# Kernel tuning notes

Hardware: AMD Instinct MI355X
Metric: run time of the kernel (lower is better)

Reference implementation:

```python
import jax, jax.numpy as jnp
import numpy as np

N_EMBD = 2048
N_Q = 32
N_KV = 8
GROUP = N_Q // N_KV   # 4
HD = N_EMBD // N_Q    # 64
BASE = 10000.0
NEG_INF = -1e30


def _rope(x):
    """Rotate-half RoPE on last dim; positions 1..t along dim -2 (as in the
    original _build_cache which uses arange(1, seq_len+1))."""
    t, d = x.shape[-2], x.shape[-1]
    d2 = d // 2
    theta = 1.0 / (BASE ** (jnp.arange(0, d, 2, dtype=jnp.float32) / d))  # (d/2,)
    pos = jnp.arange(1, t + 1, dtype=jnp.float32)                          # (t,)
    ang = pos[:, None] * theta[None, :]                                    # (t, d/2)
    ang = jnp.concatenate([ang, ang], axis=-1)                             # (t, d)
    sin, cos = jnp.sin(ang), jnp.cos(ang)
    rot = jnp.concatenate([-x[..., d2:], x[..., :d2]], axis=-1)
    return x * cos + rot * sin


def setup_inputs() -> dict:
    key = jax.random.key(0)
    ks = jax.random.split(key, 5)
    b, t = 2, 1024
    s = 1.0 / np.sqrt(N_EMBD)
    return {
        "x": jax.random.normal(ks[0], (b, t, N_EMBD), dtype=jnp.float32),
        "wq": jax.random.normal(ks[1], (N_EMBD, N_EMBD), dtype=jnp.float32) * s,
        "bq": jnp.zeros((N_EMBD,), dtype=jnp.float32),
        "wk": jax.random.normal(ks[2], (N_EMBD, N_KV * HD), dtype=jnp.float32) * s,
        "bk": jnp.zeros((N_KV * HD,), dtype=jnp.float32),
        "wv": jax.random.normal(ks[3], (N_EMBD, N_KV * HD), dtype=jnp.float32) * s,
        "bv": jnp.zeros((N_KV * HD,), dtype=jnp.float32),
        "wo": jax.random.normal(ks[4], (N_EMBD, N_EMBD), dtype=jnp.float32) * s,
        "bo": jnp.zeros((N_EMBD,), dtype=jnp.float32),
    }


def reference(x, wq, bq, wk, bk, wv, bv, wo, bo):
    b, t, _ = x.shape
    q = x @ wq + bq                                   # (b, t, E)
    k = x @ wk + bk                                   # (b, t, NKV*HD)
    v = x @ wv + bv
    q = q.reshape(b, t, N_Q, HD).transpose(0, 2, 1, 3)        # (b, nq, t, d)
    q = q.reshape(b, N_KV, GROUP, t, HD)                      # (b, hkv, g, t, d)
    k = k.reshape(b, t, N_KV, HD).transpose(0, 2, 1, 3)       # (b, hkv, t, d)
    v = v.reshape(b, t, N_KV, HD).transpose(0, 2, 1, 3)
    q = _rope(q)
    k = _rope(k)
    scale = jnp.sqrt(jnp.float32(HD))
    att = jnp.einsum("bhgqd,bhkd->bhgqk", q, k) / scale       # (b, hkv, g, t, t)
    causal = jnp.tril(jnp.ones((t, t), dtype=bool))
    att = jnp.where(causal, att, NEG_INF)
    att = jax.nn.softmax(att, axis=-1)
    out = jnp.einsum("bhgqk,bhkd->bhgqd", att, v)             # (b, hkv, g, t, d)
    out = out.transpose(0, 3, 1, 2, 4).reshape(b, t, N_EMBD)  # (b, t, E)
    return out @ wo + bo
```

## Files before the change

kernel.cpp:

```cpp
#include <hip/hip_runtime.h>
#include <hip/hip_bf16.h>
#include <cstdint>


typedef __attribute__((ext_vector_type(8))) short short8;
typedef __attribute__((ext_vector_type(4))) short short4v;
typedef __attribute__((ext_vector_type(4))) float f32x4;

__device__ inline short f2b(float f) {
  union { float f; unsigned u; } v; v.f = f;
  unsigned r = v.u + 0x7fffu + ((v.u >> 16) & 1u);
  return (short)(r >> 16);
}

__device__ inline float exp2_fast(float x) {
  float r;
  asm("v_exp_f32 %0, %1" : "=v"(r) : "v"(x));
  return r;
}

__device__ inline void gl_lds16(const void* g, void* l) {
  __builtin_amdgcn_global_load_lds((const __attribute__((address_space(1))) void*)g,
                                   (__attribute__((address_space(3))) void*)l,
                                   16, 0, 0);
}

__global__ void cast_x_kernel(const float* __restrict__ x, short* __restrict__ xb, int n4) {
  int i = blockIdx.x * 256 + threadIdx.x;
  if (i >= n4) return;
  float4 v = ((const float4*)x)[i];
  short4v o; o.x = f2b(v.x); o.y = f2b(v.y); o.z = f2b(v.z); o.w = f2b(v.w);
  ((short4v*)xb)[i] = o;
}

__global__ void wtrans_all(const float* __restrict__ wq, const float* __restrict__ wk,
                           const float* __restrict__ wv, const float* __restrict__ wo,
                           short* __restrict__ WqkvT, short* __restrict__ woT) {
  __shared__ float tile[64][65];
  const int bx = blockIdx.x;
  const float* W; short* WT; int N, off, nb;
  if (bx < 32)      { W = wq; WT = WqkvT; N = 2048; off = 0;    nb = bx * 64; }
  else if (bx < 40) { W = wk; WT = WqkvT; N = 512;  off = 2048; nb = (bx - 32) * 64; }
  else if (bx < 48) { W = wv; WT = WqkvT; N = 512;  off = 2560; nb = (bx - 40) * 64; }
  else              { W = wo; WT = woT;   N = 2048; off = 0;    nb = (bx - 48) * 64; }
  const int kb = blockIdx.y * 64;
  const int tid = threadIdx.x;
  const int c = tid & 63, r0 = tid >> 6;
#pragma unroll
  for (int s = 0; s < 16; ++s) {
    int k = r0 + s * 4;
    tile[c][k] = W[(size_t)(kb + k) * N + nb + c];
  }
  __syncthreads();
#pragma unroll
  for (int s = 0; s < 16; ++s) {
    int n = r0 + s * 4;
    WT[(size_t)(off + nb + n) * 2048 + kb + c] = f2b(tile[n][c]);
  }
}

__device__ __forceinline__ void gemm_loop_bk64(const short* __restrict__ Ag,
                                               const short* __restrict__ Bg,
                                               short* lA, short* lB,
                                               int w, int l15, int q4,
                                               f32x4 acc[2][4]) {
  const int K = 2048, NS = 32;
  auto stage = [&](int s, int d) {
    const short* As = Ag + s * 64;
    const short* Bs = Bg + s * 64;
    short* a = lA + d * 8192 + w * 512;
    gl_lds16(As, a);
    gl_lds16(As + 64 * K, a + 2048);
    gl_lds16(As + 32, a + 4096);
    gl_lds16(As + 64 * K + 32, a + 6144);
    short* bp = lB + d * 4096 + w * 512;
    gl_lds16(Bs, bp);
    gl_lds16(Bs + 32, bp + 2048);
  };
  stage(0, 0);
  for (int s = 0; s < NS; ++s) {
    const int d = s & 1;
    __syncthreads();
    if (s + 1 < NS) stage(s + 1, d ^ 1);
#pragma unroll
    for (int ks = 0; ks < 2; ++ks) {
      const short* ap = lA + d * 8192 + ks * 4096;
      const short* bp = lB + d * 4096 + ks * 2048;
      short8 af[2], bf[4];
#pragma unroll
      for (int mf = 0; mf < 2; ++mf) af[mf] = *(const short8*)(ap + (w * 32 + mf * 16 + l15) * 32 + q4 * 8);
#pragma unroll
      for (int nf = 0; nf < 4; ++nf) bf[nf] = *(const short8*)(bp + (nf * 16 + l15) * 32 + q4 * 8);
#pragma unroll
      for (int mf = 0; mf < 2; ++mf)
#pragma unroll
        for (int nf = 0; nf < 4; ++nf)
          acc[mf][nf] = __builtin_amdgcn_mfma_f32_16x16x32_bf16(af[mf], bf[nf], acc[mf][nf], 0, 0, 0);
    }
  }
}

__launch_bounds__(256, 3)
__global__ void gemm_qkv(const short* __restrict__ A, const short* __restrict__ BT,
                         const float* __restrict__ bq, const float* __restrict__ bk,
                         const float* __restrict__ bv,
                         short* __restrict__ Qb, short* __restrict__ Kb,
                         short* __restrict__ Vtd) {
  __shared__ __align__(16) short lA[16384];
  __shared__ __align__(16) short lB[8192];
  const int K = 2048;
  const int tid = threadIdx.x, lane = tid & 63, w = tid >> 6;
  const int q4 = lane >> 4, l15 = lane & 15;
  const int bn = blockIdx.x * 64, bm = blockIdx.y * 128;

  const short* Ag = A + (size_t)(bm + (tid >> 2)) * K + ((tid & 3) << 3);
  const short* Bg = BT + (size_t)(bn + (tid >> 2)) * K + ((tid & 3) << 3);

  f32x4 acc[2][4];
  const f32x4 fz = {0.f, 0.f, 0.f, 0.f};
#pragma unroll
  for (int i = 0; i < 2; ++i)
#pragma unroll
    for (int j = 0; j < 4; ++j) acc[i][j] = fz;

  gemm_loop_bk64(Ag, Bg, lA, lB, w, l15, q4, acc);

  const float L2T = 0.4152410118609203f;
  const float theta_a = exp2_fast(-(float)l15 * L2T);
  const float theta_b = exp2_fast(-(float)(l15 + 16) * L2T);
  const float s2 = 0.18033688011112042f;

  if (bn < 2048) {
    const int h = bn >> 6;
    float bb0 = bq[bn + l15], bb1 = bq[bn + 16 + l15], bb2 = bq[bn + 32 + l15], bb3 = bq[bn + 48 + l15];
#pragma unroll
    for (int mf = 0; mf < 2; ++mf)
#pragma unroll
      for (int r = 0; r < 4; ++r) {
        int row = bm + w * 32 + mf * 16 + q4 * 4 + r;
        int batch = row >> 10, t = row & 1023;
        float pos = (float)(t + 1);
        float sa, ca, sb, cb;
        __sincosf(pos * theta_a, &sa, &ca);
        __sincosf(pos * theta_b, &sb, &cb);
        float x0 = acc[mf][0][r] + bb0, x2 = acc[mf][2][r] + bb2;
        float x1 = acc[mf][1][r] + bb1, x3 = acc[mf][3][r] + bb3;
        size_t base = ((size_t)(batch * 32 + h) * 1024 + t) * 64;
        Qb[base + l15]      = f2b((x0 * ca - x2 * sa) * s2);
        Qb[base + l15 + 32] = f2b((x2 * ca + x0 * sa) * s2);
        Qb[base + l15 + 16] = f2b((x1 * cb - x3 * sb) * s2);
        Qb[base + l15 + 48] = f2b((x3 * cb + x1 * sb) * s2);
      }
  } else if (bn < 2560) {
    const int co = bn - 2048;
    const int hkv = co >> 6;
    float bb0 = bk[co + l15], bb1 = bk[co + 16 + l15], bb2 = bk[co + 32 + l15], bb3 = bk[co + 48 + l15];
#pragma unroll
    for (int mf = 0; mf < 2; ++mf)
#pragma unroll
      for (int r = 0; r < 4; ++r) {
        int row = bm + w * 32 + mf * 16 + q4 * 4 + r;
        int batch = row >> 10, t = row & 1023;
        float pos = (float)(t + 1);
        float sa, ca, sb, cb;
        __sincosf(pos * theta_a, &sa, &ca);
        __sincosf(pos * theta_b, &sb, &cb);
        float x0 = acc[mf][0][r] + bb0, x2 = acc[mf][2][r] + bb2;
        float x1 = acc[mf][1][r] + bb1, x3 = acc[mf][3][r] + bb3;
        size_t base = (size_t)(batch * 8 + hkv) * 65536 + t * 32;
        Kb[base + l15]              = f2b(x0 * ca - x2 * sa);
        Kb[base + l15 + 16]         = f2b(x1 * cb - x3 * sb);
        Kb[base + 32768 + l15]      = f2b(x2 * ca + x0 * sa);
        Kb[base + 32768 + l15 + 16] = f2b(x3 * cb + x1 * sb);
      }
  } else {
    const int co = bn - 2560;
    const int hkv = co >> 6;
    float bb[4];
#pragma unroll
    for (int nf = 0; nf < 4; ++nf) bb[nf] = bv[co + nf * 16 + l15];
#pragma unroll
    for (int mf = 0; mf < 2; ++mf)
#pragma unroll
      for (int r = 0; r < 4; ++r) {
        int row = bm + w * 32 + mf * 16 + q4 * 4 + r;
        int batch = row >> 10, t = row & 1023;
        size_t base = (size_t)(batch * 8 + hkv) * 65536 + (size_t)t * 64;
#pragma unroll
        for (int nf = 0; nf < 4; ++nf)
          Vtd[base + nf * 16 + l15] = f2b(acc[mf][nf][r] + bb[nf]);
      }
  }
}

__global__ void vtrans2_kernel(const short* __restrict__ Vtd, short* __restrict__ VTb) {
  __shared__ short tile[64][72];
  const int tt = blockIdx.x, h = blockIdx.y, b = blockIdx.z;
  const int tid = threadIdx.x;
  const size_t base = (size_t)(b * 8 + h) * 65536;
#pragma unroll
  for (int p = 0; p < 2; ++p) {
    int r = (tid >> 3) + p * 32;
    int c0 = (tid & 7) * 8;
    short8 v = *(const short8*)(Vtd + base + (size_t)(tt * 64 + r) * 64 + c0);
#pragma unroll
    for (int j = 0; j < 8; ++j) tile[c0 + j][r] = v[j];
  }
  __syncthreads();
  const int d = tid >> 2, ts = (tid & 3) * 8;
#pragma unroll
  for (int tc = 0; tc < 2; ++tc) {
    short8 v = *(const short8*)(&tile[d][tc * 32 + ts]);
    *(short8*)(VTb + base + (size_t)(tt * 2 + tc) * 2048 + d * 32 + ts) = v;
  }
}

#define PROW 72
__launch_bounds__(256, 3)
__global__ void attn5_kernel(const short* __restrict__ Qb, const short* __restrict__ Kb,
                             const short* __restrict__ VTb, short* __restrict__ AO) {
  __shared__ __align__(16) short lK[2][128 * 32];
  __shared__ __align__(16) short lVT[4][64 * 32];
  __shared__ __align__(16) short lP[4][2][16 * PROW];
  const int tid = threadIdx.x, lane = tid & 63, w = tid >> 6;
  const int q4 = lane >> 4, l15 = lane & 15;
  const int qt = (int)gridDim.x - 1 - (int)blockIdx.x;
  const int h = blockIdx.y, b = blockIdx.z;
  const int hkv = h >> 2;
  const int qb = qt * 128 + w * 32;
  const int kdiag = qb >> 6;
  const int ns = qt + 1;

  const short* Qg = Qb + (size_t)(b * 32 + h) * 65536;
  const short* Kg = Kb + (size_t)(b * 8 + hkv) * 65536;
  const short* Vg = VTb + (size_t)(b * 8 + hkv) * 65536;

  short8 qf[2][2];
#pragma unroll
  for (int mf = 0; mf < 2; ++mf) {
    const short* qr = Qg + (size_t)(qb + mf * 16 + l15) * 64 + q4 * 8;
    qf[mf][0] = *(const short8*)(qr);
    qf[mf][1] = *(const short8*)(qr + 32);
  }

  const f32x4 fz = {0.f, 0.f, 0.f, 0.f};
  f32x4 o[2][4], ol[2];
#pragma unroll
  for (int mf = 0; mf < 2; ++mf) {
    ol[mf] = fz;
#pragma unroll
    for (int i = 0; i < 4; ++i) o[mf][i] = fz;
  }
  short8 ones;
#pragma unroll
  for (int i = 0; i < 8; ++i) ones[i] = (short)0x3F80;

  for (int s = 0; s < ns; ++s) {
    {
      const short* Ksrc = Kg + (size_t)(s * 128 + (tid >> 2)) * 32 + (tid & 3) * 8;
      short* ldst = (short*)lK + w * 512;
      gl_lds16(Ksrc, ldst);
      gl_lds16(Ksrc + 64 * 32, ldst + 2048);
      gl_lds16(Ksrc + 32768, ldst + 4096);
      gl_lds16(Ksrc + 32768 + 64 * 32, ldst + 6144);
      const short* Vsrc = Vg + (size_t)(s * 4) * 2048 + tid * 8;
      short* vdst = (short*)lVT + w * 512;
#pragma unroll
      for (int c = 0; c < 4; ++c) gl_lds16(Vsrc + c * 2048, vdst + c * 2048);
    }
    __syncthreads();

#pragma unroll
    for (int ki = 0; ki < 2; ++ki) {
      const int ktg = s * 2 + ki;
      if (ktg <= kdiag) {
        short8 kf0[4], kf1[4];
#pragma unroll
        for (int nt = 0; nt < 4; ++nt) {
          kf0[nt] = *(const short8*)((short*)lK + (ki * 64 + nt * 16 + l15) * 32 + q4 * 8);
          kf1[nt] = *(const short8*)((short*)lK + 4096 + (ki * 64 + nt * 16 + l15) * 32 + q4 * 8);
        }
        const bool diag = (ktg == kdiag);
#pragma unroll
        for (int mf = 0; mf < 2; ++mf) {
          f32x4 sv[4];
#pragma unroll
          for (int nt = 0; nt < 4; ++nt) {
            f32x4 z = __builtin_amdgcn_mfma_f32_16x16x32_bf16(qf[mf][0], kf0[nt], fz, 0, 0, 0);
            sv[nt] = __builtin_amdgcn_mfma_f32_16x16x32_bf16(qf[mf][1], kf1[nt], z, 0, 0, 0);
          }
          if (diag) {
#pragma unroll
            for (int r = 0; r < 4; ++r) {
              const int qrow = qb + mf * 16 + q4 * 4 + r;
              const int col = ktg * 64 + l15;
#pragma unroll
              for (int nt = 0; nt < 4; ++nt)
                if (col + nt * 16 > qrow) sv[nt][r] = -1e30f;
            }
          }
          short* lPm = lP[w][mf];
#pragma unroll
          for (int r = 0; r < 4; ++r)
#pragma unroll
            for (int nt = 0; nt < 4; ++nt)
              lPm[(q4 * 4 + r) * PROW + nt * 16 + l15] = f2b(exp2_fast(sv[nt][r] - 16.f));
        }

        short8 vf0[4], vf1[4];
#pragma unroll
        for (int dt = 0; dt < 4; ++dt) {
          vf0[dt] = *(const short8*)((short*)lVT + (2 * ki) * 2048 + (dt * 16 + l15) * 32 + q4 * 8);
          vf1[dt] = *(const short8*)((short*)lVT + (2 * ki + 1) * 2048 + (dt * 16 + l15) * 32 + q4 * 8);
        }
#pragma unroll
        for (int mf = 0; mf < 2; ++mf) {
          const short* lPm = lP[w][mf];
          short8 pf0 = *(const short8*)(lPm + l15 * PROW + q4 * 8);
          short8 pf1 = *(const short8*)(lPm + l15 * PROW + 32 + q4 * 8);
          ol[mf] = __builtin_amdgcn_mfma_f32_16x16x32_bf16(pf0, ones, ol[mf], 0, 0, 0);
          ol[mf] = __builtin_amdgcn_mfma_f32_16x16x32_bf16(pf1, ones, ol[mf], 0, 0, 0);
#pragma unroll
          for (int dt = 0; dt < 4; ++dt) {
            o[mf][dt] = __builtin_amdgcn_mfma_f32_16x16x32_bf16(pf0, vf0[dt], o[mf][dt], 0, 0, 0);
            o[mf][dt] = __builtin_amdgcn_mfma_f32_16x16x32_bf16(pf1, vf1[dt], o[mf][dt], 0, 0, 0);
          }
        }
      }
    }
    __syncthreads();
  }

#pragma unroll
  for (int mf = 0; mf < 2; ++mf)
#pragma unroll
    for (int r = 0; r < 4; ++r) {
      float inv = __builtin_amdgcn_rcpf(ol[mf][r]);
      int row = qb + mf * 16 + q4 * 4 + r;
#pragma unroll
      for (int dt = 0; dt < 4; ++dt)
        AO[(size_t)(b * 1024 + row) * 2048 + h * 64 + dt * 16 + l15] = f2b(o[mf][dt][r] * inv);
    }
}

__launch_bounds__(256, 3)
__global__ void gemm_out(const short* __restrict__ A, const short* __restrict__ BT,
                         float* __restrict__ C, const float* __restrict__ bias,
                         int N, int K) {
  __shared__ __align__(16) short lA[16384];
  __shared__ __align__(16) short lB[8192];
  const int tid = threadIdx.x, lane = tid & 63, w = tid >> 6;
  const int q4 = lane >> 4, l15 = lane & 15;
  const int bn = blockIdx.x * 64, bm = blockIdx.y * 128;

  const short* Ag = A + (size_t)(bm + (tid >> 2)) * K + ((tid & 3) << 3);
  const short* Bg = BT + (size_t)(bn + (tid >> 2)) * K + ((tid & 3) << 3);

  f32x4 acc[2][4];
  const f32x4 fz = {0.f, 0.f, 0.f, 0.f};
#pragma unroll
  for (int i = 0; i < 2; ++i)
#pragma unroll
    for (int j = 0; j < 4; ++j) acc[i][j] = fz;

  gemm_loop_bk64(Ag, Bg, lA, lB, w, l15, q4, acc);

#pragma unroll
  for (int mf = 0; mf < 2; ++mf)
#pragma unroll
    for (int nf = 0; nf < 4; ++nf) {
      int col = bn + nf * 16 + l15;
      float bb = bias[col];
#pragma unroll
      for (int r = 0; r < 4; ++r) {
        int row = bm + w * 32 + mf * 16 + q4 * 4 + r;
        C[(size_t)row * N + col] = acc[mf][nf][r] + bb;
      }
    }
}

extern "C" void kernel_launch(void* const* d_in, const int* in_sizes, int n_in,
                              void* d_out, int out_size, void* d_ws, size_t ws_size,
                              hipStream_t stream) {
  const float* x  = (const float*)d_in[0];
  const float* wq = (const float*)d_in[1];
  const float* bq = (const float*)d_in[2];
  const float* wk = (const float*)d_in[3];
  const float* bk = (const float*)d_in[4];
  const float* wv = (const float*)d_in[5];
  const float* bv = (const float*)d_in[6];
  const float* wo = (const float*)d_in[7];
  const float* bo = (const float*)d_in[8];
  float* out = (float*)d_out;
  const int B = in_sizes[0] / (1024 * 2048);
  const int M = B * 1024;

  char* ws = (char*)d_ws;
  size_t off = 0;
  auto alloc = [&](size_t bytes) -> char* {
    char* p = ws + off;
    off += (bytes + 255) & ~(size_t)255;
    return p;
  };
  short* xb    = (short*)alloc((size_t)M * 2048 * 2);
  short* WqkvT = (short*)alloc((size_t)3072 * 2048 * 2);
  short* woT   = (short*)alloc((size_t)2048 * 2048 * 2);
  short* Qb    = (short*)alloc((size_t)B * 32 * 1024 * 64 * 2);
  short* Kb    = (short*)alloc((size_t)B * 8 * 2 * 1024 * 32 * 2);
  short* Vtd   = (short*)alloc((size_t)B * 8 * 1024 * 64 * 2);
  short* VTb   = (short*)alloc((size_t)B * 8 * 32 * 64 * 32 * 2);
  short* AO    = (short*)alloc((size_t)M * 2048 * 2);

  cast_x_kernel<<<(M * 2048 / 4 + 255) / 256, 256, 0, stream>>>(x, xb, M * 2048 / 4);
  wtrans_all<<<dim3(80, 32), 256, 0, stream>>>(wq, wk, wv, wo, WqkvT, woT);
  gemm_qkv<<<dim3(48, M / 128), 256, 0, stream>>>(xb, WqkvT, bq, bk, bv, Qb, Kb, Vtd);
  vtrans2_kernel<<<dim3(16, 8, B), 256, 0, stream>>>(Vtd, VTb);
  attn5_kernel<<<dim3(8, 32, B), 256, 0, stream>>>(Qb, Kb, VTb, AO);
  gemm_out<<<dim3(32, M / 128), 256, 0, stream>>>(AO, woT, out, bo, 2048, 2048);
}
```

Measured before the change: 209.7 us.

## Merge prep kernels, write V transposed from QKV GEMM, double-buffer attention K/V

Combines the x cast and weight transpose into a single launch. The QKV GEMM epilogue now writes V directly in the transposed tiled layout, which removes the separate vtrans kernel and its intermediate buffer. The attention kernel moves to 64-key steps with double-buffered K/V staging in LDS, so the next tile loads while the current one is computed. This uses one barrier per step instead of two. It costs twice as many iterations and uncoalesced 8-byte V stores.

```diff
diff --git a/kernel.cpp b/kernel.cpp
--- a/kernel.cpp
+++ b/kernel.cpp
@@ -25,26 +25,29 @@
                                    16, 0, 0);
 }
 
-__global__ void cast_x_kernel(const float* __restrict__ x, short* __restrict__ xb, int n4) {
-  int i = blockIdx.x * 256 + threadIdx.x;
-  if (i >= n4) return;
-  float4 v = ((const float4*)x)[i];
-  short4v o; o.x = f2b(v.x); o.y = f2b(v.y); o.z = f2b(v.z); o.w = f2b(v.w);
-  ((short4v*)xb)[i] = o;
-}
-
-__global__ void wtrans_all(const float* __restrict__ wq, const float* __restrict__ wk,
-                           const float* __restrict__ wv, const float* __restrict__ wo,
-                           short* __restrict__ WqkvT, short* __restrict__ woT) {
+__global__ void prep_kernel(const float* __restrict__ x,
+                            const float* __restrict__ wq, const float* __restrict__ wk,
+                            const float* __restrict__ wv, const float* __restrict__ wo,
+                            short* __restrict__ xb, short* __restrict__ WqkvT,
+                            short* __restrict__ woT, int nCast) {
+  const int bx = blockIdx.x;
+  const int tid = threadIdx.x;
+  if (bx < nCast) {
+    int i = bx * 256 + tid;
+    float4 v = ((const float4*)x)[i];
+    short4v o; o.x = f2b(v.x); o.y = f2b(v.y); o.z = f2b(v.z); o.w = f2b(v.w);
+    ((short4v*)xb)[i] = o;
+    return;
+  }
   __shared__ float tile[64][65];
-  const int bx = blockIdx.x;
+  const int id = bx - nCast;
+  const int wx = id % 80, ky = id / 80;
   const float* W; short* WT; int N, off, nb;
-  if (bx < 32)      { W = wq; WT = WqkvT; N = 2048; off = 0;    nb = bx * 64; }
-  else if (bx < 40) { W = wk; WT = WqkvT; N = 512;  off = 2048; nb = (bx - 32) * 64; }
-  else if (bx < 48) { W = wv; WT = WqkvT; N = 512;  off = 2560; nb = (bx - 40) * 64; }
-  else              { W = wo; WT = woT;   N = 2048; off = 0;    nb = (bx - 48) * 64; }
-  const int kb = blockIdx.y * 64;
-  const int tid = threadIdx.x;
+  if (wx < 32)      { W = wq; WT = WqkvT; N = 2048; off = 0;    nb = wx * 64; }
+  else if (wx < 40) { W = wk; WT = WqkvT; N = 512;  off = 2048; nb = (wx - 32) * 64; }
+  else if (wx < 48) { W = wv; WT = WqkvT; N = 512;  off = 2560; nb = (wx - 40) * 64; }
+  else              { W = wo; WT = woT;   N = 2048; off = 0;    nb = (wx - 48) * 64; }
+  const int kb = ky * 64;
   const int c = tid & 63, r0 = tid >> 6;
 #pragma unroll
   for (int s = 0; s < 16; ++s) {
@@ -105,7 +108,7 @@
                          const float* __restrict__ bq, const float* __restrict__ bk,
                          const float* __restrict__ bv,
                          short* __restrict__ Qb, short* __restrict__ Kb,
-                         short* __restrict__ Vtd) {
+                         short* __restrict__ VTb) {
   __shared__ __align__(16) short lA[16384];
   __shared__ __align__(16) short lB[8192];
   const int K = 2048;
@@ -180,48 +183,28 @@
 #pragma unroll
     for (int nf = 0; nf < 4; ++nf) bb[nf] = bv[co + nf * 16 + l15];
 #pragma unroll
-    for (int mf = 0; mf < 2; ++mf)
-#pragma unroll
-      for (int r = 0; r < 4; ++r) {
-        int row = bm + w * 32 + mf * 16 + q4 * 4 + r;
-        int batch = row >> 10, t = row & 1023;
-        size_t base = (size_t)(batch * 8 + hkv) * 65536 + (size_t)t * 64;
-#pragma unroll
-        for (int nf = 0; nf < 4; ++nf)
-          Vtd[base + nf * 16 + l15] = f2b(acc[mf][nf][r] + bb[nf]);
-      }
-  }
-}
-
-__global__ void vtrans2_kernel(const short* __restrict__ Vtd, short* __restrict__ VTb) {
-  __shared__ short tile[64][72];
-  const int tt = blockIdx.x, h = blockIdx.y, b = blockIdx.z;
-  const int tid = threadIdx.x;
-  const size_t base = (size_t)(b * 8 + h) * 65536;
-#pragma unroll
-  for (int p = 0; p < 2; ++p) {
-    int r = (tid >> 3) + p * 32;
-    int c0 = (tid & 7) * 8;
-    short8 v = *(const short8*)(Vtd + base + (size_t)(tt * 64 + r) * 64 + c0);
-#pragma unroll
-    for (int j = 0; j < 8; ++j) tile[c0 + j][r] = v[j];
-  }
-  __syncthreads();
-  const int d = tid >> 2, ts = (tid & 3) * 8;
-#pragma unroll
-  for (int tc = 0; tc < 2; ++tc) {
-    short8 v = *(const short8*)(&tile[d][tc * 32 + ts]);
-    *(short8*)(VTb + base + (size_t)(tt * 2 + tc) * 2048 + d * 32 + ts) = v;
+    for (int mf = 0; mf < 2; ++mf) {
+      int row0 = bm + w * 32 + mf * 16 + q4 * 4;
+      int batch = row0 >> 10, t0 = row0 & 1023;
+      size_t base = (size_t)(batch * 8 + hkv) * 65536 + (size_t)(t0 >> 5) * 2048 + (t0 & 31);
+#pragma unroll
+      for (int nf = 0; nf < 4; ++nf) {
+        short4v pk;
+#pragma unroll
+        for (int r = 0; r < 4; ++r) pk[r] = f2b(acc[mf][nf][r] + bb[nf]);
+        *(short4v*)(VTb + base + (nf * 16 + l15) * 32) = pk;
+      }
+    }
   }
 }
 
 #define PROW 72
 __launch_bounds__(256, 3)
-__global__ void attn5_kernel(const short* __restrict__ Qb, const short* __restrict__ Kb,
+__global__ void attn6_kernel(const short* __restrict__ Qb, const short* __restrict__ Kb,
                              const short* __restrict__ VTb, short* __restrict__ AO) {
-  __shared__ __align__(16) short lK[2][128 * 32];
-  __shared__ __align__(16) short lVT[4][64 * 32];
-  __shared__ __align__(16) short lP[4][2][16 * PROW];
+  __shared__ __align__(16) short lK[2][4096];
+  __shared__ __align__(16) short lV[2][4096];
+  __shared__ __align__(16) short lP[4][16 * PROW];
   const int tid = threadIdx.x, lane = tid & 63, w = tid >> 6;
   const int q4 = lane >> 4, l15 = lane & 15;
   const int qt = (int)gridDim.x - 1 - (int)blockIdx.x;
@@ -229,11 +212,12 @@
   const int hkv = h >> 2;
   const int qb = qt * 128 + w * 32;
   const int kdiag = qb >> 6;
-  const int ns = qt + 1;
+  const int ns = qt * 2 + 2;
 
   const short* Qg = Qb + (size_t)(b * 32 + h) * 65536;
   const short* Kg = Kb + (size_t)(b * 8 + hkv) * 65536;
   const short* Vg = VTb + (size_t)(b * 8 + hkv) * 65536;
+  short* lPw = lP[w];
 
   short8 qf[2][2];
 #pragma unroll
@@ -255,80 +239,71 @@
 #pragma unroll
   for (int i = 0; i < 8; ++i) ones[i] = (short)0x3F80;
 
+  auto stage = [&](int s, int d) {
+#pragma unroll
+    for (int c = 0; c < 4; ++c) {
+      int j = w * 4 + c;
+      if (j < 8) {
+        const short* src = Kg + (size_t)(j >> 2) * 32768 + s * 2048 + (j & 3) * 512 + lane * 8;
+        gl_lds16(src, &lK[d][j * 512]);
+      } else {
+        int jj = j - 8;
+        const short* src = Vg + (size_t)(s * 2 + (jj >> 2)) * 2048 + (jj & 3) * 512 + lane * 8;
+        gl_lds16(src, &lV[d][jj * 512]);
+      }
+    }
+  };
+
+  stage(0, 0);
   for (int s = 0; s < ns; ++s) {
-    {
-      const short* Ksrc = Kg + (size_t)(s * 128 + (tid >> 2)) * 32 + (tid & 3) * 8;
-      short* ldst = (short*)lK + w * 512;
-      gl_lds16(Ksrc, ldst);
-      gl_lds16(Ksrc + 64 * 32, ldst + 2048);
-      gl_lds16(Ksrc + 32768, ldst + 4096);
-      gl_lds16(Ksrc + 32768 + 64 * 32, ldst + 6144);
-      const short* Vsrc = Vg + (size_t)(s * 4) * 2048 + tid * 8;
-      short* vdst = (short*)lVT + w * 512;
-#pragma unroll
-      for (int c = 0; c < 4; ++c) gl_lds16(Vsrc + c * 2048, vdst + c * 2048);
-    }
+    const int d = s & 1;
     __syncthreads();
-
-#pragma unroll
-    for (int ki = 0; ki < 2; ++ki) {
-      const int ktg = s * 2 + ki;
-      if (ktg <= kdiag) {
-        short8 kf0[4], kf1[4];
+    if (s + 1 < ns) stage(s + 1, d ^ 1);
+    if (s <= kdiag) {
+      short8 kf0[4], kf1[4], vf0[4], vf1[4];
+#pragma unroll
+      for (int nt = 0; nt < 4; ++nt) {
+        kf0[nt] = *(const short8*)(&lK[d][(nt * 16 + l15) * 32 + q4 * 8]);
+        kf1[nt] = *(const short8*)(&lK[d][2048 + (nt * 16 + l15) * 32 + q4 * 8]);
+        vf0[nt] = *(const short8*)(&lV[d][(nt * 16 + l15) * 32 + q4 * 8]);
+        vf1[nt] = *(const short8*)(&lV[d][2048 + (nt * 16 + l15) * 32 + q4 * 8]);
+      }
+      const bool diag = (s == kdiag);
+#pragma unroll
+      for (int mf = 0; mf < 2; ++mf) {
+        f32x4 sv[4];
 #pragma unroll
         for (int nt = 0; nt < 4; ++nt) {
-          kf0[nt] = *(const short8*)((short*)lK + (ki * 64 + nt * 16 + l15) * 32 + q4 * 8);
-          kf1[nt] = *(const short8*)((short*)lK + 4096 + (ki * 64 + nt * 16 + l15) * 32 + q4 * 8);
+          f32x4 z = __builtin_amdgcn_mfma_f32_16x16x32_bf16(qf[mf][0], kf0[nt], fz, 0, 0, 0);
+          sv[nt] = __builtin_amdgcn_mfma_f32_16x16x32_bf16(qf[mf][1], kf1[nt], z, 0, 0, 0);
         }
-        const bool diag = (ktg == kdiag);
-#pragma unroll
-        for (int mf = 0; mf < 2; ++mf) {
-          f32x4 sv[4];
-#pragma unroll
-          for (int nt = 0; nt < 4; ++nt) {
-            f32x4 z = __builtin_amdgcn_mfma_f32_16x16x32_bf16(qf[mf][0], kf0[nt], fz, 0, 0, 0);
-            sv[nt] = __builtin_amdgcn_mfma_f32_16x16x32_bf16(qf[mf][1], kf1[nt], z, 0, 0, 0);
-          }
-          if (diag) {
-#pragma unroll
-            for (int r = 0; r < 4; ++r) {
-              const int qrow = qb + mf * 16 + q4 * 4 + r;
-              const int col = ktg * 64 + l15;
-#pragma unroll
-              for (int nt = 0; nt < 4; ++nt)
-                if (col + nt * 16 > qrow) sv[nt][r] = -1e30f;
-            }
-          }
-          short* lPm = lP[w][mf];
-#pragma unroll
-          for (int r = 0; r < 4; ++r)
+        if (diag) {
+#pragma unroll
+          for (int r = 0; r < 4; ++r) {
+            const int qrow = qb + mf * 16 + q4 * 4 + r;
+            const int col = s * 64 + l15;
 #pragma unroll
             for (int nt = 0; nt < 4; ++nt)
-              lPm[(q4 * 4 + r) * PROW + nt * 16 + l15] = f2b(exp2_fast(sv[nt][r] - 16.f));
-        }
-
-        short8 vf0[4], vf1[4];
-#pragma unroll
-        for (int dt = 0; dt < 4; ++dt) {
-          vf0[dt] = *(const short8*)((short*)lVT + (2 * ki) * 2048 + (dt * 16 + l15) * 32 + q4 * 8);
-          vf1[dt] = *(const short8*)((short*)lVT + (2 * ki + 1) * 2048 + (dt * 16 + l15) * 32 + q4 * 8);
-        }
-#pragma unroll
-        for (int mf = 0; mf < 2; ++mf) {
-          const short* lPm = lP[w][mf];
-          short8 pf0 = *(const short8*)(lPm + l15 * PROW + q4 * 8);
-          short8 pf1 = *(const short8*)(lPm + l15 * PROW + 32 + q4 * 8);
-          ol[mf] = __builtin_amdgcn_mfma_f32_16x16x32_bf16(pf0, ones, ol[mf], 0, 0, 0);
-          ol[mf] = __builtin_amdgcn_mfma_f32_16x16x32_bf16(pf1, ones, ol[mf], 0, 0, 0);
-#pragma unroll
-          for (int dt = 0; dt < 4; ++dt) {
-            o[mf][dt] = __builtin_amdgcn_mfma_f32_16x16x32_bf16(pf0, vf0[dt], o[mf][dt], 0, 0, 0);
-            o[mf][dt] = __builtin_amdgcn_mfma_f32_16x16x32_bf16(pf1, vf1[dt], o[mf][dt], 0, 0, 0);
+              if (col + nt * 16 > qrow) sv[nt][r] = -1e30f;
           }
         }
-      }
-    }
-    __syncthreads();
+#pragma unroll
+        for (int r = 0; r < 4; ++r)
+#pragma unroll
+          for (int nt = 0; nt < 4; ++nt)
+            lPw[(q4 * 4 + r) * PROW + nt * 16 + l15] = f2b(exp2_fast(sv[nt][r] - 16.f));
+
+        short8 pf0 = *(const short8*)(lPw + l15 * PROW + q4 * 8);
+        short8 pf1 = *(const short8*)(lPw + l15 * PROW + 32 + q4 * 8);
+        ol[mf] = __builtin_amdgcn_mfma_f32_16x16x32_bf16(pf0, ones, ol[mf], 0, 0, 0);
+        ol[mf] = __builtin_amdgcn_mfma_f32_16x16x32_bf16(pf1, ones, ol[mf], 0, 0, 0);
+#pragma unroll
+        for (int dt = 0; dt < 4; ++dt) {
+          o[mf][dt] = __builtin_amdgcn_mfma_f32_16x16x32_bf16(pf0, vf0[dt], o[mf][dt], 0, 0, 0);
+          o[mf][dt] = __builtin_amdgcn_mfma_f32_16x16x32_bf16(pf1, vf1[dt], o[mf][dt], 0, 0, 0);
+        }
+      }
+    }
   }
 
 #pragma unroll
@@ -407,14 +382,12 @@
   short* woT   = (short*)alloc((size_t)2048 * 2048 * 2);
   short* Qb    = (short*)alloc((size_t)B * 32 * 1024 * 64 * 2);
   short* Kb    = (short*)alloc((size_t)B * 8 * 2 * 1024 * 32 * 2);
-  short* Vtd   = (short*)alloc((size_t)B * 8 * 1024 * 64 * 2);
   short* VTb   = (short*)alloc((size_t)B * 8 * 32 * 64 * 32 * 2);
   short* AO    = (short*)alloc((size_t)M * 2048 * 2);
 
-  cast_x_kernel<<<(M * 2048 / 4 + 255) / 256, 256, 0, stream>>>(x, xb, M * 2048 / 4);
-  wtrans_all<<<dim3(80, 32), 256, 0, stream>>>(wq, wk, wv, wo, WqkvT, woT);
-  gemm_qkv<<<dim3(48, M / 128), 256, 0, stream>>>(xb, WqkvT, bq, bk, bv, Qb, Kb, Vtd);
-  vtrans2_kernel<<<dim3(16, 8, B), 256, 0, stream>>>(Vtd, VTb);
-  attn5_kernel<<<dim3(8, 32, B), 256, 0, stream>>>(Qb, Kb, VTb, AO);
+  const int nCast = M * 2048 / 1024;
+  prep_kernel<<<nCast + 80 * 32, 256, 0, stream>>>(x, wq, wk, wv, wo, xb, WqkvT, woT, nCast);
+  gemm_qkv<<<dim3(48, M / 128), 256, 0, stream>>>(xb, WqkvT, bq, bk, bv, Qb, Kb, VTb);
+  attn6_kernel<<<dim3(8, 32, B), 256, 0, stream>>>(Qb, Kb, VTb, AO);
   gemm_out<<<dim3(32, M / 128), 256, 0, stream>>>(AO, woT, out, bo, 2048, 2048);
 }
```

Measured after the change: 210.5 us. No clear change (+0.4%).
